# Performance work log

Measured on AMD Instinct MI355X. Metric: run time of the kernel, lower is better.

The kernel has to match this reference:

```python
import jax, jax.numpy as jnp
import numpy as np

EPS = 1e-10
COMMITMENT_COST = 0.25


def setup_inputs() -> dict:
    key = jax.random.key(0)
    k1, k2 = jax.random.split(key)
    inputs = jax.random.normal(k1, (64, 64, 32, 32), dtype=jnp.float32)
    # nn.init.uniform_(weight, -1.0, 1.0)
    embeddings = jax.random.uniform(k2, (1024, 64), dtype=jnp.float32, minval=-1.0, maxval=1.0)
    return {"inputs": inputs, "embeddings": embeddings}


def reference(inputs, embeddings):
    B, C, H, W = inputs.shape  # C == embedding_dim
    K = embeddings.shape[0]
    x = jnp.transpose(inputs, (0, 2, 3, 1)).reshape(-1, C)  # [N, D]
    d = (jnp.sum(x * x, axis=1, keepdims=True)
         - 2.0 * (x @ embeddings.T)
         + jnp.sum(embeddings * embeddings, axis=1))  # [N, K]
    idx = jnp.argmin(d, axis=1)  # [N]
    # one-hot @ embeddings == gather
    q = jnp.take(embeddings, idx, axis=0)  # [N, D]
    x4 = x.reshape(B, H, W, C)
    q4 = q.reshape(B, H, W, C)
    e_latent = jnp.mean((jax.lax.stop_gradient(q4) - x4) ** 2)
    q_latent = jnp.mean((q4 - jax.lax.stop_gradient(x4)) ** 2)
    loss = q_latent + COMMITMENT_COST * e_latent
    # straight-through estimator
    st = x4 + jax.lax.stop_gradient(q4 - x4)
    # avg_probs = mean of one-hot encodings == normalized histogram
    n = idx.shape[0]
    avg_probs = jnp.zeros((K,), dtype=jnp.float32).at[idx].add(1.0) / n
    perplexity = jnp.exp(-jnp.sum(avg_probs * jnp.log(avg_probs + EPS)))
    quantized = jnp.transpose(st, (0, 3, 1, 2))
    return quantized, loss, perplexity
```

## Files before the change

kernel.cpp:

```cpp
#include <hip/hip_runtime.h>

#define N_TOTAL   65536
#define HW_SZ     1024
#define CDIM      64
#define K_CODES   1024
#define OUT_ELEMS 4194304
#define QT        128
#define CHUNK     64
#define NCHUNK    (K_CODES / CHUNK)
#define TAU       0.004f


typedef __attribute__((ext_vector_type(8))) short short8;
typedef __attribute__((ext_vector_type(4))) float f32x4;

__device__ __forceinline__ unsigned short f2bf(float x) {
    unsigned u = __float_as_uint(x);
    return (unsigned short)((u + 0x7FFFu + ((u >> 16) & 1u)) >> 16);
}
__device__ __forceinline__ float bf2f(unsigned short h) {
    return __uint_as_float(((unsigned)h) << 16);
}
__device__ __forceinline__ void gload_lds16(const void* g, void* l) {
    __builtin_amdgcn_global_load_lds(
        (const __attribute__((address_space(1))) void*)g,
        (__attribute__((address_space(3))) void*)l, 16, 0, 0);
}

__global__ void k_prep(const float* __restrict__ emb, float* __restrict__ enorm,
                       short* __restrict__ ehi, short* __restrict__ elo,
                       unsigned int* __restrict__ hist) {
    int gid = blockIdx.x * 256 + threadIdx.x;
    float4 v = *(const float4*)(emb + gid * 4);
    float s = v.x * v.x + v.y * v.y + v.z * v.z + v.w * v.w;
#pragma unroll
    for (int off = 1; off < 16; off <<= 1) s += __shfl_xor(s, off, 64);
    if ((gid & 15) == 0) enorm[gid >> 4] = s;

    float vv[4] = {v.x, v.y, v.z, v.w};
    short h[4], l[4];
#pragma unroll
    for (int j = 0; j < 4; ++j) {
        unsigned short hh = f2bf(vv[j]);
        h[j] = (short)hh;
        l[j] = (short)f2bf(vv[j] - bf2f(hh));
    }
    *(short4*)&ehi[gid * 4] = make_short4(h[0], h[1], h[2], h[3]);
    *(short4*)&elo[gid * 4] = make_short4(l[0], l[1], l[2], l[3]);

    if (gid < K_CODES) hist[gid] = 0u;
}

__global__ __launch_bounds__(256, 2)
void k_argmin(const float* __restrict__ x, const float* __restrict__ emb,
              const short* __restrict__ ehi, const short* __restrict__ elo,
              const float* __restrict__ enorm,
              unsigned int* __restrict__ hist, float* __restrict__ partials,
              float* __restrict__ out) {
    __shared__ __align__(16) short es[2][2][CHUNK * CDIM];
    __shared__ __align__(16) short xs[2][QT * CDIM];
    __shared__ float ens[K_CODES];
    __shared__ float xnorm[QT];
    __shared__ int   oid[QT];
    __shared__ int   nflag;
    __shared__ float wdd[4];
    __shared__ int   wii[4];
    __shared__ float spw[2];

    const int tid  = threadIdx.x;
    const int lane = tid & 63;
    const int w    = tid >> 6;
    const int quad = lane >> 4;
    const int col  = lane & 15;

    const int n0  = blockIdx.x * QT;
    const int b   = n0 >> 10;
    const int hw0 = n0 & 1023;

    auto stage_async = [&](int chunk, int buf) {
        const int cbS = chunk * (CHUNK * CDIM);
#pragma unroll
        for (int h = 0; h < 2; ++h) {
            const short* tab = h ? elo : ehi;
#pragma unroll
            for (int i = 0; i < 2; ++i) {
                int s   = i * 256 + tid;
                int row = s >> 3, bb = s & 7;
                int g   = bb ^ (row & 7);
                gload_lds16(&tab[cbS + row * 64 + g * 8],
                            (void*)&es[buf][h][s * 8]);
            }
        }
    };

    if (tid < QT) xnorm[tid] = 0.f;
#pragma unroll
    for (int i = 0; i < 4; ++i) ens[i * 256 + tid] = enorm[i * 256 + tid];
    __syncthreads();

    float nloc[4] = {0.f, 0.f, 0.f, 0.f};
    const int q0s = (tid & 31) * 4;
#pragma unroll
    for (int p = 0; p < 8; ++p) {
        int c = p * 8 + (tid >> 5);
        float4 v = *(const float4*)(x + b * (CDIM * HW_SZ) + c * HW_SZ + hw0 + q0s);
        float vv[4] = {v.x, v.y, v.z, v.w};
#pragma unroll
        for (int j = 0; j < 4; ++j) {
            int q = q0s + j;
            unsigned short h = f2bf(vv[j]);
            unsigned short l = f2bf(vv[j] - bf2f(h));
            int off = q * CDIM + (((c >> 3) ^ (q & 7)) << 3) + (c & 7);
            xs[0][off] = (short)h;
            xs[1][off] = (short)l;
            nloc[j] += vv[j] * vv[j];
        }
    }
#pragma unroll
    for (int j = 0; j < 4; ++j) atomicAdd(&xnorm[q0s + j], nloc[j]);

    stage_async(0, 0);
    __syncthreads();

    short8 afr[2][2][2];
#pragma unroll
    for (int rt = 0; rt < 2; ++rt) {
        int m = w * 32 + rt * 16 + col;
#pragma unroll
        for (int kc = 0; kc < 2; ++kc) {
            int bb  = kc * 4 + quad;
            int off = m * CDIM + ((bb ^ (m & 7)) << 3);
            afr[rt][kc][0] = *(const short8*)&xs[0][off];
            afr[rt][kc][1] = *(const short8*)&xs[1][off];
        }
    }

    float d1[8], d2[8];
    int   i1[8];
#pragma unroll
    for (int t = 0; t < 8; ++t) { d1[t] = 3.4e38f; d2[t] = 3.4e38f; i1[t] = 0; }

    for (int chunk = 0; chunk < NCHUNK; ++chunk) {
        const int buf = chunk & 1;
        if (chunk) __syncthreads();
        if (chunk + 1 < NCHUNK) stage_async(chunk + 1, buf ^ 1);

#pragma unroll
        for (int ct = 0; ct < 4; ++ct) {
            const int r = ct * 16 + col;
            short8 bfr[2][2];
#pragma unroll
            for (int kc = 0; kc < 2; ++kc) {
                int bb  = kc * 4 + quad;
                int off = r * CDIM + ((bb ^ (r & 7)) << 3);
                bfr[kc][0] = *(const short8*)&es[buf][0][off];
                bfr[kc][1] = *(const short8*)&es[buf][1][off];
            }
            const int mycode = chunk * CHUNK + r;
            const float en   = ens[mycode];
#pragma unroll
            for (int rt = 0; rt < 2; ++rt) {
                f32x4 acc = {0.f, 0.f, 0.f, 0.f};
                acc = __builtin_amdgcn_mfma_f32_16x16x32_bf16(afr[rt][0][1], bfr[0][0], acc, 0, 0, 0);
                acc = __builtin_amdgcn_mfma_f32_16x16x32_bf16(afr[rt][0][0], bfr[0][1], acc, 0, 0, 0);
                acc = __builtin_amdgcn_mfma_f32_16x16x32_bf16(afr[rt][0][0], bfr[0][0], acc, 0, 0, 0);
                acc = __builtin_amdgcn_mfma_f32_16x16x32_bf16(afr[rt][1][1], bfr[1][0], acc, 0, 0, 0);
                acc = __builtin_amdgcn_mfma_f32_16x16x32_bf16(afr[rt][1][0], bfr[1][1], acc, 0, 0, 0);
                acc = __builtin_amdgcn_mfma_f32_16x16x32_bf16(afr[rt][1][0], bfr[1][0], acc, 0, 0, 0);
#pragma unroll
                for (int reg = 0; reg < 4; ++reg) {
                    int t = rt * 4 + reg;
                    float d   = __builtin_fmaf(acc[reg], -2.f, en);
                    float d1o = d1[t];
                    d2[t] = __builtin_amdgcn_fmed3f(d, d1o, d2[t]);
                    d1[t] = fminf(d, d1o);
                    i1[t] = (d < d1o) ? mycode : i1[t];
                }
            }
        }
    }

#pragma unroll
    for (int t = 0; t < 8; ++t) {
        float a1 = d1[t], a2 = d2[t];
        int ai = i1[t];
#pragma unroll
        for (int off = 1; off < 16; off <<= 1) {
            float o1 = __shfl_xor(a1, off, 64);
            float o2 = __shfl_xor(a2, off, 64);
            int   oi = __shfl_xor(ai, off, 64);
            if (o1 < a1 || (o1 == a1 && oi < ai)) {
                float loser = a1; a2 = fminf(fminf(a2, o2), loser); a1 = o1; ai = oi;
            } else {
                a2 = fminf(fminf(a2, o2), o1);
            }
        }
        d1[t] = a1; d2[t] = a2; i1[t] = ai;
    }

    float* rd1   = (float*)xs;
    float* rd2   = rd1 + QT;
    int*   ri    = (int*)(rd2 + QT);
    int*   flist = (int*)((char*)xs + 1536);
    float* xqf   = (float*)((char*)xs + 2048);
    float* tile  = (float*)((char*)xs + 2560);

    __syncthreads();
    if (tid == 0) nflag = 0;
    if (col == 0) {
#pragma unroll
        for (int rt = 0; rt < 2; ++rt)
#pragma unroll
            for (int reg = 0; reg < 4; ++reg) {
                int t = rt * 4 + reg;
                int m = w * 32 + rt * 16 + quad * 4 + reg;
                rd1[m] = d1[t];
                rd2[m] = d2[t];
                ri [m] = i1[t];
            }
    }
    __syncthreads();

    if (tid < QT) {
        if (rd2[tid] - rd1[tid] < TAU) {
            int slot = atomicAdd(&nflag, 1);
            flist[slot] = tid;
        }
    }
    __syncthreads();

    for (int f = 0; f < nflag; ++f) {
        const int q = flist[f];
        if (tid < CDIM) xqf[tid] = x[b * (CDIM * HW_SZ) + tid * HW_SZ + hw0 + q];
        __syncthreads();
        float dm = 3.4e38f; int im = 0;
#pragma unroll
        for (int cd = 0; cd < 4; ++cd) {
            const int k = tid + cd * 256;
            const float4* er = (const float4*)(emb + k * CDIM);
            const float4* xr = (const float4*)xqf;
            float dot = 0.f;
#pragma unroll
            for (int c4 = 0; c4 < 16; ++c4) {
                float4 e = er[c4], xv = xr[c4];
                dot += e.x * xv.x + e.y * xv.y + e.z * xv.z + e.w * xv.w;
            }
            float d = ens[k] - 2.f * dot;
            if (d < dm) { dm = d; im = k; }
        }
#pragma unroll
        for (int off = 1; off < 64; off <<= 1) {
            float od = __shfl_xor(dm, off, 64);
            int   oi = __shfl_xor(im, off, 64);
            if (od < dm || (od == dm && oi < im)) { dm = od; im = oi; }
        }
        if (lane == 0) { wdd[w] = dm; wii[w] = im; }
        __syncthreads();
        if (tid == 0) {
            float bd = wdd[0]; int bi = wii[0];
#pragma unroll
            for (int ww = 1; ww < 4; ++ww)
                if (wdd[ww] < bd || (wdd[ww] == bd && wii[ww] < bi)) { bd = wdd[ww]; bi = wii[ww]; }
            rd1[q] = bd; ri[q] = bi;
        }
        __syncthreads();
    }

    if (tid < QT) {
        int ai = ri[tid];
        oid[tid] = ai;
        atomicAdd(&hist[ai], 1u);
        float sp = rd1[tid] + xnorm[tid];
#pragma unroll
        for (int off = 32; off; off >>= 1) sp += __shfl_down(sp, off, 64);
        if (lane == 0) spw[tid >> 6] = sp;
    }
    __syncthreads();
    if (tid == 0) partials[blockIdx.x] = spw[0] + spw[1];

#pragma unroll
    for (int h = 0; h < 2; ++h) {
        {
            int q = tid >> 2, j = tid & 3;
            int code = oid[h * 64 + q];
            short8 hi0 = *(const short8*)&ehi[code * CDIM + j * 16];
            short8 hi1 = *(const short8*)&ehi[code * CDIM + j * 16 + 8];
            short8 lo0 = *(const short8*)&elo[code * CDIM + j * 16];
            short8 lo1 = *(const short8*)&elo[code * CDIM + j * 16 + 8];
            float* dst = &tile[q * 72 + j * 16];
#pragma unroll
            for (int k = 0; k < 8; ++k) {
                dst[k]     = bf2f((unsigned short)hi0[k]) + bf2f((unsigned short)lo0[k]);
                dst[8 + k] = bf2f((unsigned short)hi1[k]) + bf2f((unsigned short)lo1[k]);
            }
        }
        __syncthreads();
        {
            int c = tid >> 2;
            float* ob = out + b * (CDIM * HW_SZ) + c * HW_SZ + hw0 + h * 64;
#pragma unroll
            for (int p = 0; p < 4; ++p) {
                int q = ((tid & 3) + p * 4) * 4;
                float4 v;
                v.x = tile[(q + 0) * 72 + c];
                v.y = tile[(q + 1) * 72 + c];
                v.z = tile[(q + 2) * 72 + c];
                v.w = tile[(q + 3) * 72 + c];
                *(float4*)&ob[q] = v;
            }
        }
        if (h == 0) __syncthreads();
    }
}

__global__ void k_final(const float* __restrict__ partials,
                        const unsigned int* __restrict__ hist,
                        float* __restrict__ out) {
    int tid = threadIdx.x;
    float ss = 0.f;
#pragma unroll
    for (int i = 0; i < 2; ++i) ss += partials[i * 256 + tid];
    float s = 0.f;
#pragma unroll
    for (int i = 0; i < 4; ++i) {
        float p = (float)hist[i * 256 + tid] * (1.0f / 65536.0f);
        s += p * logf(p + 1e-10f);
    }
    __shared__ float fin[8];
#pragma unroll
    for (int off = 32; off; off >>= 1) {
        ss += __shfl_down(ss, off, 64);
        s  += __shfl_down(s, off, 64);
    }
    if ((tid & 63) == 0) { fin[tid >> 6] = ss; fin[4 + (tid >> 6)] = s; }
    __syncthreads();
    if (tid == 0) {
        float sse = fin[0] + fin[1] + fin[2] + fin[3];
        float ent = fin[4] + fin[5] + fin[6] + fin[7];
        out[OUT_ELEMS]     = 1.25f * sse * (1.0f / (float)OUT_ELEMS);
        out[OUT_ELEMS + 1] = expf(-ent);
    }
}

extern "C" void kernel_launch(void* const* d_in, const int* in_sizes, int n_in,
                              void* d_out, int out_size, void* d_ws, size_t ws_size,
                              hipStream_t stream) {
    const float* x   = (const float*)d_in[0];
    const float* emb = (const float*)d_in[1];
    float* out = (float*)d_out;
    char* ws = (char*)d_ws;
    float*        enorm    = (float*)(ws);
    unsigned int* hist     = (unsigned int*)(ws + 4096);
    short*        ehi      = (short*)(ws + 12288);
    short*        elo      = (short*)(ws + 143360);
    float*        partials = (float*)(ws + 274432);

    k_prep  <<<64, 256, 0, stream>>>(emb, enorm, ehi, elo, hist);
    k_argmin<<<N_TOTAL / QT, 256, 0, stream>>>(x, emb, ehi, elo, enorm, hist, partials, out);
    k_final <<<1, 256, 0, stream>>>(partials, hist, out);
}
```

Before: 151.3 us.

## Halve query tile, load x fragments directly to registers, raise occupancy

Shrinks the per-block query tile from 128 to 64 rows, so each wave handles one 16-row MFMA tile instead of two. The x tile is no longer staged through LDS: each lane loads its A fragments straight from global memory and splits them into bf16 hi/lo. enorm moves into LDS through an async global-to-LDS load, and the epilogue reuses the embedding LDS buffer. Launch bounds go to 4 blocks per CU to hide latency, at the cost of each codebook chunk being reused by half as many queries and twice as many blocks reloading the codebook.

```diff
diff --git a/kernel.cpp b/kernel.cpp
--- a/kernel.cpp
+++ b/kernel.cpp
@@ -5,7 +5,7 @@
 #define CDIM      64
 #define K_CODES   1024
 #define OUT_ELEMS 4194304
-#define QT        128
+#define QT        64
 #define CHUNK     64
 #define NCHUNK    (K_CODES / CHUNK)
 #define TAU       0.004f
@@ -51,21 +51,18 @@
     if (gid < K_CODES) hist[gid] = 0u;
 }
 
-__global__ __launch_bounds__(256, 2)
+__global__ __launch_bounds__(256, 4)
 void k_argmin(const float* __restrict__ x, const float* __restrict__ emb,
               const short* __restrict__ ehi, const short* __restrict__ elo,
               const float* __restrict__ enorm,
               unsigned int* __restrict__ hist, float* __restrict__ partials,
               float* __restrict__ out) {
     __shared__ __align__(16) short es[2][2][CHUNK * CDIM];
-    __shared__ __align__(16) short xs[2][QT * CDIM];
-    __shared__ float ens[K_CODES];
+    __shared__ __align__(16) float ens[K_CODES];
     __shared__ float xnorm[QT];
-    __shared__ int   oid[QT];
     __shared__ int   nflag;
     __shared__ float wdd[4];
     __shared__ int   wii[4];
-    __shared__ float spw[2];
 
     const int tid  = threadIdx.x;
     const int lane = tid & 63;
@@ -93,52 +90,34 @@
         }
     };
 
-    if (tid < QT) xnorm[tid] = 0.f;
-#pragma unroll
-    for (int i = 0; i < 4; ++i) ens[i * 256 + tid] = enorm[i * 256 + tid];
-    __syncthreads();
-
-    float nloc[4] = {0.f, 0.f, 0.f, 0.f};
-    const int q0s = (tid & 31) * 4;
-#pragma unroll
-    for (int p = 0; p < 8; ++p) {
-        int c = p * 8 + (tid >> 5);
-        float4 v = *(const float4*)(x + b * (CDIM * HW_SZ) + c * HW_SZ + hw0 + q0s);
-        float vv[4] = {v.x, v.y, v.z, v.w};
-#pragma unroll
-        for (int j = 0; j < 4; ++j) {
-            int q = q0s + j;
-            unsigned short h = f2bf(vv[j]);
-            unsigned short l = f2bf(vv[j] - bf2f(h));
-            int off = q * CDIM + (((c >> 3) ^ (q & 7)) << 3) + (c & 7);
-            xs[0][off] = (short)h;
-            xs[1][off] = (short)l;
-            nloc[j] += vv[j] * vv[j];
-        }
-    }
-#pragma unroll
-    for (int j = 0; j < 4; ++j) atomicAdd(&xnorm[q0s + j], nloc[j]);
-
     stage_async(0, 0);
-    __syncthreads();
-
-    short8 afr[2][2][2];
-#pragma unroll
-    for (int rt = 0; rt < 2; ++rt) {
-        int m = w * 32 + rt * 16 + col;
-#pragma unroll
-        for (int kc = 0; kc < 2; ++kc) {
-            int bb  = kc * 4 + quad;
-            int off = m * CDIM + ((bb ^ (m & 7)) << 3);
-            afr[rt][kc][0] = *(const short8*)&xs[0][off];
-            afr[rt][kc][1] = *(const short8*)&xs[1][off];
-        }
-    }
-
-    float d1[8], d2[8];
-    int   i1[8];
-#pragma unroll
-    for (int t = 0; t < 8; ++t) { d1[t] = 3.4e38f; d2[t] = 3.4e38f; i1[t] = 0; }
+    gload_lds16(&enorm[tid * 4], (void*)&ens[tid * 4]);
+
+    const float* xb = x + b * (CDIM * HW_SZ) + hw0 + w * 16 + col;
+    short8 afr[2][2];
+    float nloc = 0.f;
+#pragma unroll
+    for (int kc = 0; kc < 2; ++kc) {
+#pragma unroll
+        for (int j = 0; j < 8; ++j) {
+            int c = (kc * 4 + quad) * 8 + j;
+            float v = xb[c * HW_SZ];
+            unsigned short h = f2bf(v);
+            afr[kc][0][j] = (short)h;
+            afr[kc][1][j] = (short)f2bf(v - bf2f(h));
+            nloc = __builtin_fmaf(v, v, nloc);
+        }
+    }
+    nloc += __shfl_xor(nloc, 16, 64);
+    nloc += __shfl_xor(nloc, 32, 64);
+    if (quad == 0) xnorm[w * 16 + col] = nloc;
+
+    __syncthreads();
+
+    float d1[4], d2[4];
+    int   i1[4];
+#pragma unroll
+    for (int t = 0; t < 4; ++t) { d1[t] = 3.4e38f; d2[t] = 3.4e38f; i1[t] = 0; }
 
     for (int chunk = 0; chunk < NCHUNK; ++chunk) {
         const int buf = chunk & 1;
@@ -158,30 +137,27 @@
             }
             const int mycode = chunk * CHUNK + r;
             const float en   = ens[mycode];
-#pragma unroll
-            for (int rt = 0; rt < 2; ++rt) {
-                f32x4 acc = {0.f, 0.f, 0.f, 0.f};
-                acc = __builtin_amdgcn_mfma_f32_16x16x32_bf16(afr[rt][0][1], bfr[0][0], acc, 0, 0, 0);
-                acc = __builtin_amdgcn_mfma_f32_16x16x32_bf16(afr[rt][0][0], bfr[0][1], acc, 0, 0, 0);
-                acc = __builtin_amdgcn_mfma_f32_16x16x32_bf16(afr[rt][0][0], bfr[0][0], acc, 0, 0, 0);
-                acc = __builtin_amdgcn_mfma_f32_16x16x32_bf16(afr[rt][1][1], bfr[1][0], acc, 0, 0, 0);
-                acc = __builtin_amdgcn_mfma_f32_16x16x32_bf16(afr[rt][1][0], bfr[1][1], acc, 0, 0, 0);
-                acc = __builtin_amdgcn_mfma_f32_16x16x32_bf16(afr[rt][1][0], bfr[1][0], acc, 0, 0, 0);
-#pragma unroll
-                for (int reg = 0; reg < 4; ++reg) {
-                    int t = rt * 4 + reg;
-                    float d   = __builtin_fmaf(acc[reg], -2.f, en);
-                    float d1o = d1[t];
-                    d2[t] = __builtin_amdgcn_fmed3f(d, d1o, d2[t]);
-                    d1[t] = fminf(d, d1o);
-                    i1[t] = (d < d1o) ? mycode : i1[t];
-                }
-            }
-        }
-    }
-
-#pragma unroll
-    for (int t = 0; t < 8; ++t) {
+
+            f32x4 acc = {0.f, 0.f, 0.f, 0.f};
+            acc = __builtin_amdgcn_mfma_f32_16x16x32_bf16(afr[0][1], bfr[0][0], acc, 0, 0, 0);
+            acc = __builtin_amdgcn_mfma_f32_16x16x32_bf16(afr[0][0], bfr[0][1], acc, 0, 0, 0);
+            acc = __builtin_amdgcn_mfma_f32_16x16x32_bf16(afr[0][0], bfr[0][0], acc, 0, 0, 0);
+            acc = __builtin_amdgcn_mfma_f32_16x16x32_bf16(afr[1][1], bfr[1][0], acc, 0, 0, 0);
+            acc = __builtin_amdgcn_mfma_f32_16x16x32_bf16(afr[1][0], bfr[1][1], acc, 0, 0, 0);
+            acc = __builtin_amdgcn_mfma_f32_16x16x32_bf16(afr[1][0], bfr[1][0], acc, 0, 0, 0);
+#pragma unroll
+            for (int reg = 0; reg < 4; ++reg) {
+                float d   = __builtin_fmaf(acc[reg], -2.f, en);
+                float d1o = d1[reg];
+                d2[reg] = __builtin_amdgcn_fmed3f(d, d1o, d2[reg]);
+                d1[reg] = fminf(d, d1o);
+                i1[reg] = (d < d1o) ? mycode : i1[reg];
+            }
+        }
+    }
+
+#pragma unroll
+    for (int t = 0; t < 4; ++t) {
         float a1 = d1[t], a2 = d2[t];
         int ai = i1[t];
 #pragma unroll
@@ -198,26 +174,23 @@
         d1[t] = a1; d2[t] = a2; i1[t] = ai;
     }
 
-    float* rd1   = (float*)xs;
+    float* rd1   = (float*)es;
     float* rd2   = rd1 + QT;
     int*   ri    = (int*)(rd2 + QT);
-    int*   flist = (int*)((char*)xs + 1536);
-    float* xqf   = (float*)((char*)xs + 2048);
-    float* tile  = (float*)((char*)xs + 2560);
+    int*   flist = (int*)((char*)es + 768);
+    float* xqf   = (float*)((char*)es + 1024);
+    float* tile  = (float*)((char*)es + 1280);
 
     __syncthreads();
     if (tid == 0) nflag = 0;
     if (col == 0) {
 #pragma unroll
-        for (int rt = 0; rt < 2; ++rt)
-#pragma unroll
-            for (int reg = 0; reg < 4; ++reg) {
-                int t = rt * 4 + reg;
-                int m = w * 32 + rt * 16 + quad * 4 + reg;
-                rd1[m] = d1[t];
-                rd2[m] = d2[t];
-                ri [m] = i1[t];
-            }
+        for (int reg = 0; reg < 4; ++reg) {
+            int m = w * 16 + quad * 4 + reg;
+            rd1[m] = d1[reg];
+            rd2[m] = d2[reg];
+            ri [m] = i1[reg];
+        }
     }
     __syncthreads();
 
@@ -268,48 +241,41 @@
 
     if (tid < QT) {
         int ai = ri[tid];
-        oid[tid] = ai;
         atomicAdd(&hist[ai], 1u);
         float sp = rd1[tid] + xnorm[tid];
 #pragma unroll
         for (int off = 32; off; off >>= 1) sp += __shfl_down(sp, off, 64);
-        if (lane == 0) spw[tid >> 6] = sp;
-    }
-    __syncthreads();
-    if (tid == 0) partials[blockIdx.x] = spw[0] + spw[1];
-
-#pragma unroll
-    for (int h = 0; h < 2; ++h) {
-        {
-            int q = tid >> 2, j = tid & 3;
-            int code = oid[h * 64 + q];
-            short8 hi0 = *(const short8*)&ehi[code * CDIM + j * 16];
-            short8 hi1 = *(const short8*)&ehi[code * CDIM + j * 16 + 8];
-            short8 lo0 = *(const short8*)&elo[code * CDIM + j * 16];
-            short8 lo1 = *(const short8*)&elo[code * CDIM + j * 16 + 8];
-            float* dst = &tile[q * 72 + j * 16];
-#pragma unroll
-            for (int k = 0; k < 8; ++k) {
-                dst[k]     = bf2f((unsigned short)hi0[k]) + bf2f((unsigned short)lo0[k]);
-                dst[8 + k] = bf2f((unsigned short)hi1[k]) + bf2f((unsigned short)lo1[k]);
-            }
-        }
-        __syncthreads();
-        {
-            int c = tid >> 2;
-            float* ob = out + b * (CDIM * HW_SZ) + c * HW_SZ + hw0 + h * 64;
-#pragma unroll
-            for (int p = 0; p < 4; ++p) {
-                int q = ((tid & 3) + p * 4) * 4;
-                float4 v;
-                v.x = tile[(q + 0) * 72 + c];
-                v.y = tile[(q + 1) * 72 + c];
-                v.z = tile[(q + 2) * 72 + c];
-                v.w = tile[(q + 3) * 72 + c];
-                *(float4*)&ob[q] = v;
-            }
-        }
-        if (h == 0) __syncthreads();
+        if (tid == 0) partials[blockIdx.x] = sp;
+    }
+
+    {
+        int q = tid >> 2, j = tid & 3;
+        int code = ri[q];
+        short8 hi0 = *(const short8*)&ehi[code * CDIM + j * 16];
+        short8 hi1 = *(const short8*)&ehi[code * CDIM + j * 16 + 8];
+        short8 lo0 = *(const short8*)&elo[code * CDIM + j * 16];
+        short8 lo1 = *(const short8*)&elo[code * CDIM + j * 16 + 8];
+        float* dst = &tile[q * 72 + j * 16];
+#pragma unroll
+        for (int k = 0; k < 8; ++k) {
+            dst[k]     = bf2f((unsigned short)hi0[k]) + bf2f((unsigned short)lo0[k]);
+            dst[8 + k] = bf2f((unsigned short)hi1[k]) + bf2f((unsigned short)lo1[k]);
+        }
+    }
+    __syncthreads();
+    {
+        int c = tid >> 2;
+        float* ob = out + b * (CDIM * HW_SZ) + c * HW_SZ + hw0;
+#pragma unroll
+        for (int p = 0; p < 4; ++p) {
+            int q = ((tid & 3) + p * 4) * 4;
+            float4 v;
+            v.x = tile[(q + 0) * 72 + c];
+            v.y = tile[(q + 1) * 72 + c];
+            v.z = tile[(q + 2) * 72 + c];
+            v.w = tile[(q + 3) * 72 + c];
+            *(float4*)&ob[q] = v;
+        }
     }
 }
 
@@ -319,7 +285,7 @@
     int tid = threadIdx.x;
     float ss = 0.f;
 #pragma unroll
-    for (int i = 0; i < 2; ++i) ss += partials[i * 256 + tid];
+    for (int i = 0; i < 4; ++i) ss += partials[i * 256 + tid];
     float s = 0.f;
 #pragma unroll
     for (int i = 0; i < 4; ++i) {
@@ -351,9 +317,9 @@
     char* ws = (char*)d_ws;
     float*        enorm    = (float*)(ws);
     unsigned int* hist     = (unsigned int*)(ws + 4096);
+    float*        partials = (float*)(ws + 8192);
     short*        ehi      = (short*)(ws + 12288);
     short*        elo      = (short*)(ws + 143360);
-    float*        partials = (float*)(ws + 274432);
 
     k_prep  <<<64, 256, 0, stream>>>(emb, enorm, ehi, elo, hist);
     k_argmin<<<N_TOTAL / QT, 256, 0, stream>>>(x, emb, ehi, elo, enorm, hist, partials, out);
```

New measurement: 175.4 us. 15.9% more time.
